# Optimization experiments

Hardware: AMD Instinct MI355X
Metric: run time of the kernel (lower is better)

Reference implementation:

```python
import jax, jax.numpy as jnp
import numpy as np

N_NODES = 50000
N_EDGES = 1200000
N_REL = 45
IN_C, HID_C, OUT_C = 64, 32, 16


def setup_inputs() -> dict:
    key = jax.random.key(0)
    ks = jax.random.split(key, 9)
    x = jax.random.normal(ks[0], (N_NODES, IN_C), dtype=jnp.float32)
    edge_index = jax.random.randint(ks[1], (2, N_EDGES), 0, N_NODES, dtype=jnp.int64)
    edge_type = jax.random.randint(ks[2], (N_EDGES,), 0, N_REL, dtype=jnp.int64)
    s = 0.05
    W1 = jax.random.normal(ks[3], (N_REL, IN_C, HID_C), dtype=jnp.float32) * s
    root1 = jax.random.normal(ks[4], (IN_C, HID_C), dtype=jnp.float32) * s
    b1 = jax.random.normal(ks[5], (HID_C,), dtype=jnp.float32) * s
    W2 = jax.random.normal(ks[6], (N_REL, HID_C, OUT_C), dtype=jnp.float32) * s
    root2 = jax.random.normal(ks[7], (HID_C, OUT_C), dtype=jnp.float32) * s
    b2 = jax.random.normal(ks[8], (OUT_C,), dtype=jnp.float32) * s
    return {"x": x, "edge_index": edge_index, "edge_type": edge_type,
            "W1": W1, "root1": root1, "b1": b1,
            "W2": W2, "root2": root2, "b2": b2}


def rgcn_conv(x, edge_index, edge_type, W, root, b):
    # PyG RGCNConv: out_i = x_i @ root + b + sum_r mean_{j in N_r(i)} (x_j @ W_r)
    N = x.shape[0]
    R = W.shape[0]
    src, dst = edge_index[0], edge_index[1]
    # per-relation transform of all nodes: [R, N, out]
    h = jnp.einsum('ni,rio->rno', x, W)
    # per-edge message: gather transformed src feature for edge's relation
    msg = h[edge_type, src]                      # [E, out]
    # segment id combines (relation, dst) for per-relation mean aggregation
    seg = edge_type * N + dst                    # [E]
    sums = jax.ops.segment_sum(msg, seg, num_segments=R * N)        # [R*N, out]
    cnt = jax.ops.segment_sum(jnp.ones((msg.shape[0],), x.dtype), seg,
                              num_segments=R * N)                   # [R*N]
    mean = sums / jnp.maximum(cnt, 1.0)[:, None]
    agg = mean.reshape(R, N, -1).sum(axis=0)     # sum over relations -> [N, out]
    return agg + x @ root + b


def reference(x, edge_index, edge_type, W1, root1, b1, W2, root2, b2):
    h = rgcn_conv(x, edge_index, edge_type, W1, root1, b1)
    h = jax.nn.relu(h)
    out = rgcn_conv(h, edge_index, edge_type, W2, root2, b2)
    return out
```

## Files before the change

kernel.cpp:

```cpp
#include <hip/hip_runtime.h>
#include <hip/hip_fp16.h>
#include <cstdint>
#include <cstddef>

#define NN   50000
#define NE   1200000
#define NR   45
#define INC  64
#define HIDC 32
#define OUTC 16
#define NSG  13
#define NBKT (NSG * NR)
#define MAXE (NE + NBKT * 64)
#define NCHUNK (MAXE / 64)
#define EPB 4096
#define NB  ((NE + EPB - 1) / EPB)
#define QDW 6250
#define QDD 12500
#define NTILE ((NN + 255) / 256)


typedef _Float16 f16x8 __attribute__((ext_vector_type(8)));
typedef float    f32x4 __attribute__((ext_vector_type(4)));

union F16Bits { unsigned short u; _Float16 f; };
union ABFrag   { uint4 u; f16x8 f; };

__global__ __launch_bounds__(256) void preph_k(const float* __restrict__ W1,
                                               const float* __restrict__ W2,
                                               const float* __restrict__ x,
                                               const int* __restrict__ ei,
                                               const int* __restrict__ et,
                                               const float* __restrict__ root1,
                                               const float* __restrict__ root2,
                                               const float* __restrict__ b1,
                                               __half* __restrict__ W1f,
                                               __half* __restrict__ W2f,
                                               __half* __restrict__ xh,
                                               float2* __restrict__ rootp1,
                                               float2* __restrict__ rootp2,
                                               float2* __restrict__ b1p,
                                               unsigned* __restrict__ ghist,
                                               unsigned* __restrict__ rsorted,
                                               unsigned* __restrict__ flagbuf) {
    __shared__ unsigned lh[NBKT];
    int t = threadIdx.x, b = blockIdx.x;
    for (int i = t; i < NBKT; i += 256) lh[i] = 0;
    __syncthreads();
    if (b < NB) {
        #pragma unroll
        for (int it = 0; it < EPB / 256; ++it) {
            int e = b * EPB + it * 256 + t;
            if (e < NE) {
                int r = et[e], src = ei[e], dst = ei[NE + e];
                if ((unsigned)r < NR && (unsigned)src < NN && (unsigned)dst < NN)
                    atomicAdd(&lh[(src >> 12) * NR + r], 1u);
            }
        }
    }
    __syncthreads();
    if (b < NB)
        for (int i = t; i < NBKT; i += 256) ghist[(size_t)i * NB + b] = lh[i];
    int g = b * 256 + t;
    int gthreads = gridDim.x * 256;
    for (int i = g; i < MAXE; i += gthreads) rsorted[i] = 0xFFFFFFFFu;
    if (b == 0) flagbuf[t] = 0;
    if (g < NR * 2048) {
        int r = g >> 11, rem = g & 2047;
        int kb = rem >> 10, nb = (rem >> 9) & 1;
        int lane = (rem >> 3) & 63, j = rem & 7;
        int k = kb * 32 + (lane >> 4) * 8 + j;
        int n = nb * 16 + (lane & 15);
        W1f[g] = __float2half(W1[(r * INC + k) * HIDC + n]);
    }
    if (g < NR * 512) {
        int r = g >> 9, rem = g & 511;
        int lane = (rem >> 3) & 63, j = rem & 7;
        int k = (lane >> 4) * 8 + j;
        int kc = (k >> 1) + ((k & 1) << 4);
        int n = lane & 15;
        W2f[g] = __float2half(W2[(r * HIDC + kc) * OUTC + n]);
    }
    if (g < NN * INC / 2) {
        float2 f = ((const float2*)x)[g];
        union { __half2 h; unsigned u; } cv;
        cv.h = __floats2half2_rn(f.x, f.y);
        ((unsigned*)xh)[g] = cv.u;
    }
    if (g < 1024) {
        int in = g >> 4, w = g & 15;
        rootp1[g] = make_float2(root1[in * HIDC + w], root1[in * HIDC + w + 16]);
    }
    if (g < 256) {
        int in = g >> 3, w = g & 7;
        rootp2[g] = make_float2(root2[in * OUTC + w], root2[in * OUTC + w + 8]);
    }
    if (g < 16) b1p[g] = make_float2(b1[g], b1[g + 16]);
}

__global__ __launch_bounds__(64) void scanA_k(const unsigned* __restrict__ ghist,
                                              unsigned* __restrict__ bbase,
                                              unsigned* __restrict__ btot) {
    int b = blockIdx.x, j = threadIdx.x;
    const unsigned* __restrict__ row = ghist + (size_t)b * NB;
    unsigned* __restrict__ orow = bbase + (size_t)b * NB;
    unsigned v[5], s = 0;
    #pragma unroll
    for (int k = 0; k < 5; ++k) {
        int idx = j * 5 + k;
        v[k] = (idx < NB) ? row[idx] : 0u;
        s += v[k];
    }
    unsigned inc = s;
    #pragma unroll
    for (int off = 1; off < 64; off <<= 1) {
        unsigned n = __shfl_up(inc, off);
        if (j >= off) inc += n;
    }
    unsigned run = inc - s;
    #pragma unroll
    for (int k = 0; k < 5; ++k) {
        int idx = j * 5 + k;
        if (idx < NB) orow[idx] = run;
        run += v[k];
    }
    if (j == 63) btot[b] = inc;
}

__global__ __launch_bounds__(1024) void scanB_k(const unsigned* __restrict__ btot,
                                                unsigned* __restrict__ gbase,
                                                int* __restrict__ chunkrel) {
    __shared__ unsigned tot[NBKT];
    __shared__ unsigned gb[NBKT + 1];
    int t = threadIdx.x;
    for (int i = t; i < NBKT; i += 1024) tot[i] = btot[i];
    __syncthreads();
    if (t == 0) {
        unsigned acc = 0;
        for (int i = 0; i < NBKT; ++i) {
            gb[i] = acc;
            acc += (tot[i] + 63u) & ~63u;
        }
        gb[NBKT] = acc;
    }
    __syncthreads();
    for (int i = t; i <= NBKT; i += 1024) gbase[i] = gb[i];
    for (int c = t; c < NCHUNK; c += 1024) {
        unsigned pos = (unsigned)c << 6;
        int lo = 0, hi = NBKT - 1;
        while (lo < hi) {
            int mid = (lo + hi + 1) >> 1;
            if (gb[mid] <= pos) lo = mid; else hi = mid - 1;
        }
        chunkrel[c] = lo % NR;
    }
}

__global__ __launch_bounds__(1024) void scat_k(const int* __restrict__ ei,
                                               const int* __restrict__ et,
                                               const unsigned* __restrict__ bbase,
                                               const unsigned* __restrict__ gbase,
                                               unsigned* __restrict__ rsorted) {
    __shared__ unsigned lbase[NBKT], lcur[NBKT];
    int t = threadIdx.x, bx = blockIdx.x;
    for (int i = t; i < NBKT; i += 1024) {
        lbase[i] = gbase[i] + bbase[(size_t)i * NB + bx];
        lcur[i] = 0;
    }
    __syncthreads();
    #pragma unroll
    for (int it = 0; it < EPB / 1024; ++it) {
        int e = bx * EPB + it * 1024 + t;
        if (e < NE) {
            int r = et[e], src = ei[e], dst = ei[NE + e];
            if ((unsigned)r < NR && (unsigned)src < NN && (unsigned)dst < NN) {
                int bkt = (src >> 12) * NR + r;
                unsigned local = atomicAdd(&lcur[bkt], 1u);
                rsorted[lbase[bkt] + local] = (unsigned)src | ((unsigned)dst << 16);
            }
        }
    }
}

__global__ __launch_bounds__(1024) void relcnt_k(const unsigned* __restrict__ rsorted,
                                                 const unsigned* __restrict__ gbase,
                                                 unsigned short* __restrict__ cnt16,
                                                 unsigned short* __restrict__ rank16) {
    __shared__ unsigned lds[QDW];
    int r = blockIdx.x >> 2, q = blockIdx.x & 3, t = threadIdx.x;
    unsigned dlo = q * QDD, dhi = dlo + QDD;
    for (int w = t; w < QDW; w += 1024) lds[w] = 0;
    __syncthreads();
    for (int sg = 0; sg < NSG; ++sg) {
        unsigned base = gbase[sg * NR + r], end = gbase[sg * NR + r + 1];
        for (unsigned s = base + t; s < end; s += 1024) {
            unsigned d = rsorted[s] >> 16;
            if (d >= dlo && d < dhi) {
                unsigned off = d - dlo;
                unsigned old = atomicAdd(&lds[off >> 1], (off & 1) ? 0x10000u : 1u);
                rank16[s] = (unsigned short)((off & 1) ? (old >> 16) : (old & 0xFFFFu));
            }
        }
    }
    __syncthreads();
    unsigned* __restrict__ cp = (unsigned*)(cnt16 + (size_t)r * NN + dlo);
    for (int w = t; w < QDW; w += 1024) cp[w] = lds[w];
}

__global__ __launch_bounds__(256) void dp_k(const unsigned short* __restrict__ cnt16,
                                            unsigned* __restrict__ packed,
                                            unsigned* __restrict__ rowptr,
                                            unsigned* __restrict__ flags) {
    __shared__ unsigned wsum[4];
    __shared__ unsigned excl_s;
    int t = threadIdx.x, b = blockIdx.x;
    int lane = t & 63, wv = t >> 6;
    int dst = b * 256 + t;
    unsigned deg = 0;
    if (dst < NN) {
        unsigned run = 0;
        #pragma unroll 5
        for (int r = 0; r < NR; ++r) {
            unsigned c = cnt16[(size_t)r * NN + dst];
            F16Bits fb; fb.f = (_Float16)(c ? 1.0f / (float)c : 0.0f);
            packed[(size_t)r * NN + dst] = (run & 0xFFFFu) | ((unsigned)fb.u << 16);
            run += c;
        }
        deg = run;
    }
    unsigned s = deg;
    #pragma unroll
    for (int off = 1; off < 64; off <<= 1) {
        unsigned n = __shfl_up(s, off);
        if (lane >= off) s += n;
    }
    if (lane == 63) wsum[wv] = s;
    __syncthreads();
    unsigned waveoff = 0;
    if (wv > 0) waveoff += wsum[0];
    if (wv > 1) waveoff += wsum[1];
    if (wv > 2) waveoff += wsum[2];
    unsigned blockT = wsum[0] + wsum[1] + wsum[2] + wsum[3];
    unsigned local_excl = waveoff + s - deg;
    if (t == 0) {
        if (b == 0) {
            excl_s = 0;
            atomicExch(&flags[0], 0x80000000u | blockT);
        } else {
            atomicExch(&flags[b], 0x40000000u | blockT);
            unsigned ex = 0;
            int p = b - 1;
            while (p >= 0) {
                unsigned f = atomicAdd(&flags[p], 0u);
                unsigned st = f >> 30;
                if (st == 0) continue;
                ex += f & 0x3FFFFFFFu;
                if (st >= 2) break;
                --p;
            }
            excl_s = ex;
            atomicExch(&flags[b], 0x80000000u | (ex + blockT));
        }
    }
    __syncthreads();
    unsigned ex = excl_s;
    if (dst < NN) rowptr[dst] = ex + local_excl;
    if (b == (int)gridDim.x - 1 && t == 0) rowptr[NN] = ex + blockT;
}

__global__ __launch_bounds__(256) void finalize_k(const unsigned* __restrict__ rsorted,
                                                  const unsigned short* __restrict__ rank16,
                                                  const unsigned* __restrict__ packed,
                                                  const unsigned* __restrict__ rowptr,
                                                  const int* __restrict__ chunkrel,
                                                  uint2* __restrict__ pedges) {
    int s = blockIdx.x * 256 + threadIdx.x;
    if (s >= MAXE) return;
    unsigned v = rsorted[s];
    unsigned dst = v >> 16;
    if (dst >= NN) { pedges[s] = make_uint2(0u, 0x80000000u); return; }
    int r = chunkrel[s >> 6];
    unsigned pk = packed[(size_t)r * NN + dst];
    unsigned dpos = rowptr[dst] + (pk & 0xFFFFu) + (unsigned)rank16[s];
    pedges[s] = make_uint2((v & 0xFFFFu) | (pk & 0xFFFF0000u),
                           dpos | ((unsigned)r << 25));
}

__global__ __launch_bounds__(256) void msg1_k(const __half* __restrict__ xh,
                                              const __half* __restrict__ W1f,
                                              const uint2* __restrict__ pedges,
                                              __half* __restrict__ msg) {
    int tid = threadIdx.x;
    int lane = tid & 63;
    int wave = (blockIdx.x * 256 + tid) >> 6;
    if (wave >= NCHUNK) return;
    int e = (wave << 6) + lane;
    uint2 er = pedges[e];
    int w1 = (int)er.y;
    int rel = __builtin_amdgcn_readfirstlane((w1 >> 25) & 63);
    F16Bits fb; fb.u = (unsigned short)(er.x >> 16);
    float sc = (float)fb.f;
    int src = er.x & 0xFFFF;
    int drow = (w1 < 0) ? NE : (w1 & 0x1FFFFFF);
    const uint4* __restrict__ wf = (const uint4*)W1f + (size_t)rel * 256;
    ABFrag b00, b01, b10, b11;
    b00.u = wf[0 * 64 + lane];
    b01.u = wf[1 * 64 + lane];
    b10.u = wf[2 * 64 + lane];
    b11.u = wf[3 * 64 + lane];
    int quad = lane >> 4, col = lane & 15;
    ABFrag a0[4], a1[4];
    #pragma unroll
    for (int tl = 0; tl < 4; ++tl) {
        int s = __shfl(src, tl * 16 + col);
        const uint4* __restrict__ xp = (const uint4*)(xh + (size_t)s * INC) + quad;
        a0[tl].u = xp[0];
        a1[tl].u = xp[4];
    }
    #pragma unroll
    for (int tl = 0; tl < 4; ++tl) {
        f32x4 acc0 = {0.f, 0.f, 0.f, 0.f}, acc1 = {0.f, 0.f, 0.f, 0.f};
        acc0 = __builtin_amdgcn_mfma_f32_16x16x32_f16(a0[tl].f, b00.f, acc0, 0, 0, 0);
        acc0 = __builtin_amdgcn_mfma_f32_16x16x32_f16(a1[tl].f, b10.f, acc0, 0, 0, 0);
        acc1 = __builtin_amdgcn_mfma_f32_16x16x32_f16(a0[tl].f, b01.f, acc1, 0, 0, 0);
        acc1 = __builtin_amdgcn_mfma_f32_16x16x32_f16(a1[tl].f, b11.f, acc1, 0, 0, 0);
        #pragma unroll
        for (int i = 0; i < 4; ++i) {
            int ee = tl * 16 + quad * 4 + i;
            int dr   = __shfl(drow, ee);
            float si = __shfl(sc, ee);
            union { __half2 h; unsigned u; } cv;
            cv.h = __floats2half2_rn(acc0[i] * si, acc1[i] * si);
            ((unsigned*)(msg + (size_t)dr * HIDC))[col] = cv.u;
        }
    }
}

__global__ __launch_bounds__(256) void msg2_k(const __half* __restrict__ hh,
                                              const __half* __restrict__ W2f,
                                              const uint2* __restrict__ pedges,
                                              __half* __restrict__ msg) {
    int tid = threadIdx.x;
    int lane = tid & 63;
    int wave = (blockIdx.x * 256 + tid) >> 6;
    if (wave >= NCHUNK) return;
    int e = (wave << 6) + lane;
    uint2 er = pedges[e];
    int w1 = (int)er.y;
    int rel = __builtin_amdgcn_readfirstlane((w1 >> 25) & 63);
    F16Bits fb; fb.u = (unsigned short)(er.x >> 16);
    float sc = (float)fb.f;
    int src = er.x & 0xFFFF;
    int drow = (w1 < 0) ? NE : (w1 & 0x1FFFFFF);
    ABFrag bf;
    bf.u = ((const uint4*)W2f + (size_t)rel * 64)[lane];
    int quad = lane >> 4, col = lane & 15;
    ABFrag a[4];
    #pragma unroll
    for (int tl = 0; tl < 4; ++tl) {
        int s = __shfl(src, tl * 16 + col);
        a[tl].u = *((const uint4*)(hh + (size_t)s * HIDC) + quad);
    }
    #pragma unroll
    for (int tl = 0; tl < 4; ++tl) {
        f32x4 acc = {0.f, 0.f, 0.f, 0.f};
        acc = __builtin_amdgcn_mfma_f32_16x16x32_f16(a[tl].f, bf.f, acc, 0, 0, 0);
        #pragma unroll
        for (int i = 0; i < 4; ++i) {
            int ee = tl * 16 + quad * 4 + i;
            int dr   = __shfl(drow, ee);
            float si = __shfl(sc, ee);
            float v  = acc[i] * si;
            float p  = __shfl_xor(v, 8);
            if (col < 8) {
                union { __half2 h; unsigned u; } cv;
                cv.h = __floats2half2_rn(v, p);
                ((unsigned*)(msg + (size_t)dr * OUTC))[col] = cv.u;
            }
        }
    }
}

__global__ __launch_bounds__(256) void gather1_k(const __half* __restrict__ xh,
                                                 const float2* __restrict__ rootp1,
                                                 const float2* __restrict__ b1p,
                                                 const __half* __restrict__ msg,
                                                 const unsigned* __restrict__ rowptr,
                                                 __half* __restrict__ hh) {
    int tid = threadIdx.x;
    int lane = tid & 63;
    int wid = (blockIdx.x * 256 + tid) >> 6;
    int g = lane >> 2, j = lane & 3;
    unsigned k0 = rowptr[wid], k1 = rowptr[wid + 1];
    float2 rw[4][4];
    #pragma unroll
    for (int i = 0; i < 4; ++i) {
        const float4* __restrict__ rp =
            (const float4*)rootp1 + ((4 * g + i) << 3) + 2 * j;
        float4 u0 = rp[0], u1 = rp[1];
        rw[i][0] = make_float2(u0.x, u0.y);
        rw[i][1] = make_float2(u0.z, u0.w);
        rw[i][2] = make_float2(u1.x, u1.y);
        rw[i][3] = make_float2(u1.z, u1.w);
    }
    float acc[8] = {0.f, 0.f, 0.f, 0.f, 0.f, 0.f, 0.f, 0.f};
    for (unsigned k = k0 + g; k < k1; k += 16) {
        uint4 v = ((const uint4*)(msg + (size_t)k * HIDC))[j];
        union { unsigned u; __half2 h; } c0, c1, c2, c3;
        c0.u = v.x; c1.u = v.y; c2.u = v.z; c3.u = v.w;
        float2 f0 = __half22float2(c0.h), f1 = __half22float2(c1.h);
        float2 f2 = __half22float2(c2.h), f3 = __half22float2(c3.h);
        acc[0] += f0.x; acc[1] += f0.y;
        acc[2] += f1.x; acc[3] += f1.y;
        acc[4] += f2.x; acc[5] += f2.y;
        acc[6] += f3.x; acc[7] += f3.y;
    }
    union { uint2 u; __half2 h[2]; } xv;
    xv.u = ((const uint2*)(xh + (size_t)wid * INC))[g];
    float2 xa = __half22float2(xv.h[0]), xb = __half22float2(xv.h[1]);
    float xs[4] = { xa.x, xa.y, xb.x, xb.y };
    #pragma unroll
    for (int i = 0; i < 4; ++i) {
        #pragma unroll
        for (int q = 0; q < 4; ++q) {
            acc[2 * q]     = fmaf(xs[i], rw[i][q].x, acc[2 * q]);
            acc[2 * q + 1] = fmaf(xs[i], rw[i][q].y, acc[2 * q + 1]);
        }
    }
    #pragma unroll
    for (int off = 4; off < 64; off <<= 1) {
        #pragma unroll
        for (int q = 0; q < 8; ++q) acc[q] += __shfl_xor(acc[q], off);
    }
    if (g == 0) {
        const float4* __restrict__ bp4 = (const float4*)b1p;
        float4 bb0 = bp4[2 * j], bb1 = bp4[2 * j + 1];
        float2 bq[4] = { make_float2(bb0.x, bb0.y), make_float2(bb0.z, bb0.w),
                         make_float2(bb1.x, bb1.y), make_float2(bb1.z, bb1.w) };
        unsigned um[4];
        #pragma unroll
        for (int q = 0; q < 4; ++q) {
            float vx = acc[2 * q] + bq[q].x, vy = acc[2 * q + 1] + bq[q].y;
            union { __half2 h2; unsigned u; } cv;
            cv.h2 = __floats2half2_rn(vx > 0.f ? vx : 0.f, vy > 0.f ? vy : 0.f);
            um[q] = cv.u;
        }
        ((uint4*)(hh + (size_t)wid * HIDC))[j] = make_uint4(um[0], um[1], um[2], um[3]);
    }
}

__global__ __launch_bounds__(256) void gather2_k(const __half* __restrict__ hh,
                                                 const float2* __restrict__ rootp2,
                                                 const float* __restrict__ b2,
                                                 const __half* __restrict__ msg,
                                                 const unsigned* __restrict__ rowptr,
                                                 float* __restrict__ out) {
    int tid = threadIdx.x;
    int lane = tid & 63;
    int wid = (blockIdx.x * 256 + tid) >> 6;
    int g = lane >> 1, j = lane & 1;
    unsigned k0 = rowptr[wid], k1 = rowptr[wid + 1];
    const float4* __restrict__ rp = (const float4*)rootp2 + (g << 2) + 2 * j;
    float4 u0 = rp[0], u1 = rp[1];
    float2 rw[4] = { make_float2(u0.x, u0.y), make_float2(u0.z, u0.w),
                     make_float2(u1.x, u1.y), make_float2(u1.z, u1.w) };
    float acc[8] = {0.f, 0.f, 0.f, 0.f, 0.f, 0.f, 0.f, 0.f};
    for (unsigned k = k0 + g; k < k1; k += 32) {
        uint4 v = ((const uint4*)(msg + (size_t)k * OUTC))[j];
        union { unsigned u; __half2 h; } c0, c1, c2, c3;
        c0.u = v.x; c1.u = v.y; c2.u = v.z; c3.u = v.w;
        float2 f0 = __half22float2(c0.h), f1 = __half22float2(c1.h);
        float2 f2 = __half22float2(c2.h), f3 = __half22float2(c3.h);
        acc[0] += f0.x; acc[1] += f0.y;
        acc[2] += f1.x; acc[3] += f1.y;
        acc[4] += f2.x; acc[5] += f2.y;
        acc[6] += f3.x; acc[7] += f3.y;
    }
    unsigned hw = ((const unsigned*)(hh + (size_t)wid * HIDC))[g & 15];
    union { unsigned u; __half2 h; } hc; hc.u = hw;
    float2 hf = __half22float2(hc.h);
    float hv = (g < 16) ? hf.x : hf.y;
    #pragma unroll
    for (int q = 0; q < 4; ++q) {
        acc[2 * q]     = fmaf(hv, rw[q].x, acc[2 * q]);
        acc[2 * q + 1] = fmaf(hv, rw[q].y, acc[2 * q + 1]);
    }
    #pragma unroll
    for (int off = 2; off < 64; off <<= 1) {
        #pragma unroll
        for (int q = 0; q < 8; ++q) acc[q] += __shfl_xor(acc[q], off);
    }
    if (g == 0) {
        float* __restrict__ orow = out + (size_t)wid * OUTC;
        float4 ba = ((const float4*)b2)[j];
        float4 bb = ((const float4*)b2)[j + 2];
        ((float4*)orow)[j] = make_float4(acc[0] + ba.x, acc[2] + ba.y,
                                         acc[4] + ba.z, acc[6] + ba.w);
        ((float4*)orow)[j + 2] = make_float4(acc[1] + bb.x, acc[3] + bb.y,
                                             acc[5] + bb.z, acc[7] + bb.w);
    }
}

extern "C" void kernel_launch(void* const* d_in, const int* in_sizes, int n_in,
                              void* d_out, int out_size, void* d_ws, size_t ws_size,
                              hipStream_t stream) {
    const float* x     = (const float*)d_in[0];
    const int*   ei    = (const int*)d_in[1];
    const int*   et    = (const int*)d_in[2];
    const float* W1    = (const float*)d_in[3];
    const float* root1 = (const float*)d_in[4];
    const float* b1    = (const float*)d_in[5];
    const float* W2    = (const float*)d_in[6];
    const float* root2 = (const float*)d_in[7];
    const float* b2    = (const float*)d_in[8];
    float* out = (float*)d_out;

    char* ws = (char*)d_ws;
    size_t o = 0;
    auto alloc = [&](size_t bytes) -> char* {
        char* p = ws + o;
        o = (o + bytes + 255) & ~(size_t)255;
        return p;
    };
    unsigned* rsorted = (unsigned*)alloc((size_t)MAXE * 4);
    unsigned* flagbuf = (unsigned*)alloc(256 * 4);
    unsigned* ghist   = (unsigned*)alloc((size_t)NBKT * NB * 4);
    unsigned* bbase   = (unsigned*)alloc((size_t)NBKT * NB * 4);
    unsigned* btot    = (unsigned*)alloc((size_t)NBKT * 4);
    unsigned* gbase   = (unsigned*)alloc((size_t)(NBKT + 1) * 4);
    int*      chunkrel= (int*)     alloc((size_t)NCHUNK * 4);
    unsigned short* rank16 = (unsigned short*)alloc((size_t)MAXE * 2);
    unsigned short* cnt16  = (unsigned short*)alloc((size_t)NR * NN * 2);
    unsigned* packed  = (unsigned*)alloc((size_t)NR * NN * 4);
    unsigned* rowptr  = (unsigned*)alloc(((size_t)NN + 1) * 4);
    uint2*    pedges  = (uint2*)   alloc((size_t)MAXE * 8);
    __half*   W1f     = (__half*)  alloc((size_t)NR * 2048 * 2);
    __half*   W2f     = (__half*)  alloc((size_t)NR * 512 * 2);
    __half*   xh      = (__half*)  alloc((size_t)NN * INC * 2);
    __half*   hh      = (__half*)  alloc((size_t)NN * HIDC * 2);
    float2*   rootp1  = (float2*)  alloc(1024 * 8);
    float2*   rootp2  = (float2*)  alloc(256 * 8);
    float2*   b1p     = (float2*)  alloc(16 * 8);
    char*     msgraw  = alloc(((size_t)NE + 1) * 64);
    __half*   msg1    = (__half*)msgraw;
    __half*   msg2    = (__half*)msgraw;

    int prep_grid = NN * INC / 2 / 256;
    preph_k   <<<prep_grid, 256, 0, stream>>>(W1, W2, x, ei, et, root1, root2, b1,
                                              W1f, W2f, xh, rootp1, rootp2, b1p,
                                              ghist, rsorted, flagbuf);
    scanA_k   <<<NBKT, 64, 0, stream>>>(ghist, bbase, btot);
    scanB_k   <<<1, 1024, 0, stream>>>(btot, gbase, chunkrel);
    scat_k    <<<NB, 1024, 0, stream>>>(ei, et, bbase, gbase, rsorted);
    relcnt_k  <<<4 * NR, 1024, 0, stream>>>(rsorted, gbase, cnt16, rank16);
    dp_k      <<<NTILE, 256, 0, stream>>>(cnt16, packed, rowptr, flagbuf + 32);
    finalize_k<<<(MAXE + 255) / 256, 256, 0, stream>>>(rsorted, rank16, packed,
                                                       rowptr, chunkrel, pedges);
    msg1_k    <<<(MAXE + 255) / 256, 256, 0, stream>>>(xh, W1f, pedges, msg1);
    gather1_k <<<NN * 64 / 256, 256, 0, stream>>>(xh, rootp1, b1p, msg1, rowptr, hh);
    msg2_k    <<<(MAXE + 255) / 256, 256, 0, stream>>>(hh, W2f, pedges, msg2);
    gather2_k <<<NN * 64 / 256, 256, 0, stream>>>(hh, rootp2, b2, msg2, rowptr, out);
}
```

Measured before the change: 296.7 us.

## Fuse edge finalize into message kernels and widen message stores to 16 bytes

Removes the finalize kernel and the pedges buffer; msg1 and msg2 now compute the destination row, scale and source directly from rsorted, rank16, packed and rowptr. Message writes are rearranged with lane shuffles so each lane stores a full uint4 per row instead of scattered 4-byte stores. This saves one launch and a write plus two reads of an 8-byte-per-edge buffer. In exchange, the packed/rowptr/rank16 lookups are repeated in both message kernels, and the extra shuffles and selects add ALU work.

Result: slower. 310.6 us (+4.7%).

```diff
diff --git a/kernel.cpp b/kernel.cpp
--- a/kernel.cpp
+++ b/kernel.cpp
@@ -268,40 +268,32 @@
     if (b == (int)gridDim.x - 1 && t == 0) rowptr[NN] = ex + blockT;
 }
 
-__global__ __launch_bounds__(256) void finalize_k(const unsigned* __restrict__ rsorted,
-                                                  const unsigned short* __restrict__ rank16,
-                                                  const unsigned* __restrict__ packed,
-                                                  const unsigned* __restrict__ rowptr,
-                                                  const int* __restrict__ chunkrel,
-                                                  uint2* __restrict__ pedges) {
-    int s = blockIdx.x * 256 + threadIdx.x;
-    if (s >= MAXE) return;
-    unsigned v = rsorted[s];
-    unsigned dst = v >> 16;
-    if (dst >= NN) { pedges[s] = make_uint2(0u, 0x80000000u); return; }
-    int r = chunkrel[s >> 6];
-    unsigned pk = packed[(size_t)r * NN + dst];
-    unsigned dpos = rowptr[dst] + (pk & 0xFFFFu) + (unsigned)rank16[s];
-    pedges[s] = make_uint2((v & 0xFFFFu) | (pk & 0xFFFF0000u),
-                           dpos | ((unsigned)r << 25));
-}
-
 __global__ __launch_bounds__(256) void msg1_k(const __half* __restrict__ xh,
                                               const __half* __restrict__ W1f,
-                                              const uint2* __restrict__ pedges,
+                                              const unsigned* __restrict__ rsorted,
+                                              const unsigned short* __restrict__ rank16,
+                                              const unsigned* __restrict__ packed,
+                                              const unsigned* __restrict__ rowptr,
+                                              const int* __restrict__ chunkrel,
                                               __half* __restrict__ msg) {
     int tid = threadIdx.x;
     int lane = tid & 63;
     int wave = (blockIdx.x * 256 + tid) >> 6;
     if (wave >= NCHUNK) return;
     int e = (wave << 6) + lane;
-    uint2 er = pedges[e];
-    int w1 = (int)er.y;
-    int rel = __builtin_amdgcn_readfirstlane((w1 >> 25) & 63);
-    F16Bits fb; fb.u = (unsigned short)(er.x >> 16);
-    float sc = (float)fb.f;
-    int src = er.x & 0xFFFF;
-    int drow = (w1 < 0) ? NE : (w1 & 0x1FFFFFF);
+    int rel = __builtin_amdgcn_readfirstlane(chunkrel[wave]);
+    unsigned v = rsorted[e];
+    unsigned dst = v >> 16;
+    int src = 0, drow = NE;
+    float sc = 0.f;
+    if (dst < NN) {
+        unsigned pk = packed[(size_t)rel * NN + dst];
+        unsigned dpos = rowptr[dst] + (pk & 0xFFFFu) + (unsigned)rank16[e];
+        src = v & 0xFFFF;
+        F16Bits fb; fb.u = (unsigned short)(pk >> 16);
+        sc = (float)fb.f;
+        drow = (int)dpos;
+    }
     const uint4* __restrict__ wf = (const uint4*)W1f + (size_t)rel * 256;
     ABFrag b00, b01, b10, b11;
     b00.u = wf[0 * 64 + lane];
@@ -317,6 +309,7 @@
         a0[tl].u = xp[0];
         a1[tl].u = xp[4];
     }
+    int eloc = lane >> 2, wq = lane & 3, isel = eloc & 3;
     #pragma unroll
     for (int tl = 0; tl < 4; ++tl) {
         f32x4 acc0 = {0.f, 0.f, 0.f, 0.f}, acc1 = {0.f, 0.f, 0.f, 0.f};
@@ -324,34 +317,57 @@
         acc0 = __builtin_amdgcn_mfma_f32_16x16x32_f16(a1[tl].f, b10.f, acc0, 0, 0, 0);
         acc1 = __builtin_amdgcn_mfma_f32_16x16x32_f16(a0[tl].f, b01.f, acc1, 0, 0, 0);
         acc1 = __builtin_amdgcn_mfma_f32_16x16x32_f16(a1[tl].f, b11.f, acc1, 0, 0, 0);
+        unsigned um[4];
         #pragma unroll
         for (int i = 0; i < 4; ++i) {
             int ee = tl * 16 + quad * 4 + i;
-            int dr   = __shfl(drow, ee);
             float si = __shfl(sc, ee);
             union { __half2 h; unsigned u; } cv;
             cv.h = __floats2half2_rn(acc0[i] * si, acc1[i] * si);
-            ((unsigned*)(msg + (size_t)dr * HIDC))[col] = cv.u;
-        }
+            um[i] = cv.u;
+        }
+        unsigned w4[4];
+        #pragma unroll
+        for (int q = 0; q < 4; ++q) {
+            int srcl = ((lane >> 4) << 4) + (wq << 2) + q;
+            unsigned t0 = __shfl(um[0], srcl);
+            unsigned t1 = __shfl(um[1], srcl);
+            unsigned t2 = __shfl(um[2], srcl);
+            unsigned t3 = __shfl(um[3], srcl);
+            w4[q] = (isel == 0) ? t0 : (isel == 1) ? t1 : (isel == 2) ? t2 : t3;
+        }
+        int dr = __shfl(drow, tl * 16 + eloc);
+        ((uint4*)(msg + (size_t)dr * HIDC))[wq] =
+            make_uint4(w4[0], w4[1], w4[2], w4[3]);
     }
 }
 
 __global__ __launch_bounds__(256) void msg2_k(const __half* __restrict__ hh,
                                               const __half* __restrict__ W2f,
-                                              const uint2* __restrict__ pedges,
+                                              const unsigned* __restrict__ rsorted,
+                                              const unsigned short* __restrict__ rank16,
+                                              const unsigned* __restrict__ packed,
+                                              const unsigned* __restrict__ rowptr,
+                                              const int* __restrict__ chunkrel,
                                               __half* __restrict__ msg) {
     int tid = threadIdx.x;
     int lane = tid & 63;
     int wave = (blockIdx.x * 256 + tid) >> 6;
     if (wave >= NCHUNK) return;
     int e = (wave << 6) + lane;
-    uint2 er = pedges[e];
-    int w1 = (int)er.y;
-    int rel = __builtin_amdgcn_readfirstlane((w1 >> 25) & 63);
-    F16Bits fb; fb.u = (unsigned short)(er.x >> 16);
-    float sc = (float)fb.f;
-    int src = er.x & 0xFFFF;
-    int drow = (w1 < 0) ? NE : (w1 & 0x1FFFFFF);
+    int rel = __builtin_amdgcn_readfirstlane(chunkrel[wave]);
+    unsigned v = rsorted[e];
+    unsigned dst = v >> 16;
+    int src = 0, drow = NE;
+    float sc = 0.f;
+    if (dst < NN) {
+        unsigned pk = packed[(size_t)rel * NN + dst];
+        unsigned dpos = rowptr[dst] + (pk & 0xFFFFu) + (unsigned)rank16[e];
+        src = v & 0xFFFF;
+        F16Bits fb; fb.u = (unsigned short)(pk >> 16);
+        sc = (float)fb.f;
+        drow = (int)dpos;
+    }
     ABFrag bf;
     bf.u = ((const uint4*)W2f + (size_t)rel * 64)[lane];
     int quad = lane >> 4, col = lane & 15;
@@ -361,22 +377,36 @@
         int s = __shfl(src, tl * 16 + col);
         a[tl].u = *((const uint4*)(hh + (size_t)s * HIDC) + quad);
     }
+    int isel2 = (lane >> 1) & 3;
     #pragma unroll
     for (int tl = 0; tl < 4; ++tl) {
         f32x4 acc = {0.f, 0.f, 0.f, 0.f};
         acc = __builtin_amdgcn_mfma_f32_16x16x32_f16(a[tl].f, bf.f, acc, 0, 0, 0);
+        unsigned um[4];
         #pragma unroll
         for (int i = 0; i < 4; ++i) {
             int ee = tl * 16 + quad * 4 + i;
-            int dr   = __shfl(drow, ee);
             float si = __shfl(sc, ee);
-            float v  = acc[i] * si;
-            float p  = __shfl_xor(v, 8);
-            if (col < 8) {
-                union { __half2 h; unsigned u; } cv;
-                cv.h = __floats2half2_rn(v, p);
-                ((unsigned*)(msg + (size_t)dr * OUTC))[col] = cv.u;
-            }
+            float vv = acc[i] * si;
+            float p  = __shfl_xor(vv, 8);
+            union { __half2 h; unsigned u; } cv;
+            cv.h = __floats2half2_rn(vv, p);
+            um[i] = cv.u;
+        }
+        unsigned w4[4];
+        #pragma unroll
+        for (int q = 0; q < 4; ++q) {
+            int srcl = (((lane >> 3) << 4) + ((lane & 1) << 2) + q) & 63;
+            unsigned t0 = __shfl(um[0], srcl);
+            unsigned t1 = __shfl(um[1], srcl);
+            unsigned t2 = __shfl(um[2], srcl);
+            unsigned t3 = __shfl(um[3], srcl);
+            w4[q] = (isel2 == 0) ? t0 : (isel2 == 1) ? t1 : (isel2 == 2) ? t2 : t3;
+        }
+        int dr = __shfl(drow, (tl * 16 + (lane >> 1)) & 63);
+        if (lane < 32) {
+            ((uint4*)(msg + (size_t)dr * OUTC))[lane & 1] =
+                make_uint4(w4[0], w4[1], w4[2], w4[3]);
         }
     }
 }
@@ -533,7 +563,6 @@
     unsigned short* cnt16  = (unsigned short*)alloc((size_t)NR * NN * 2);
     unsigned* packed  = (unsigned*)alloc((size_t)NR * NN * 4);
     unsigned* rowptr  = (unsigned*)alloc(((size_t)NN + 1) * 4);
-    uint2*    pedges  = (uint2*)   alloc((size_t)MAXE * 8);
     __half*   W1f     = (__half*)  alloc((size_t)NR * 2048 * 2);
     __half*   W2f     = (__half*)  alloc((size_t)NR * 512 * 2);
     __half*   xh      = (__half*)  alloc((size_t)NN * INC * 2);
@@ -554,10 +583,12 @@
     scat_k    <<<NB, 1024, 0, stream>>>(ei, et, bbase, gbase, rsorted);
     relcnt_k  <<<4 * NR, 1024, 0, stream>>>(rsorted, gbase, cnt16, rank16);
     dp_k      <<<NTILE, 256, 0, stream>>>(cnt16, packed, rowptr, flagbuf + 32);
-    finalize_k<<<(MAXE + 255) / 256, 256, 0, stream>>>(rsorted, rank16, packed,
-                                                       rowptr, chunkrel, pedges);
-    msg1_k    <<<(MAXE + 255) / 256, 256, 0, stream>>>(xh, W1f, pedges, msg1);
+    msg1_k    <<<(MAXE + 255) / 256, 256, 0, stream>>>(xh, W1f, rsorted, rank16,
+                                                       packed, rowptr, chunkrel,
+                                                       msg1);
     gather1_k <<<NN * 64 / 256, 256, 0, stream>>>(xh, rootp1, b1p, msg1, rowptr, hh);
-    msg2_k    <<<(MAXE + 255) / 256, 256, 0, stream>>>(hh, W2f, pedges, msg2);
+    msg2_k    <<<(MAXE + 255) / 256, 256, 0, stream>>>(hh, W2f, rsorted, rank16,
+                                                       packed, rowptr, chunkrel,
+                                                       msg2);
     gather2_k <<<NN * 64 / 256, 256, 0, stream>>>(hh, rootp2, b2, msg2, rowptr, out);
 }
```
